# Optimization experiments

Hardware: AMD Instinct MI355X
Metric: run time of the kernel (lower is better)

The kernel has to match this reference:

```python
import jax, jax.numpy as jnp
import numpy as np

B, L, DIN = 2048, 70, 15
HID, NF, K = 16, 4, 40          # hidden_units//2, n_features, kernel_size
C = DIN + 1 + NF                # 20 signature input channels (original + time + conv features)
Z0 = 64
SIG_CH = C + C * C + C ** 3     # 8420, depth-3 signature channels


def setup_inputs() -> dict:
    key = jax.random.key(0)
    ks = jax.random.split(key, 8)
    return {
        "observed_data": jax.random.normal(ks[0], (B, L, DIN), jnp.float32),
        "observed_tp": jnp.linspace(0.0, 1.0, L, dtype=jnp.float32),
        "conv1_w": jax.random.normal(ks[1], (HID, DIN, K), jnp.float32) / np.float32(np.sqrt(DIN * K)),
        "conv1_b": jnp.zeros((HID,), jnp.float32),
        "conv2_w": jax.random.normal(ks[2], (HID, HID), jnp.float32) / np.float32(np.sqrt(HID)),
        "conv2_b": jnp.zeros((HID,), jnp.float32),
        "conv3_w": jax.random.normal(ks[3], (NF, HID), jnp.float32) / np.float32(np.sqrt(HID)),
        "conv3_b": jnp.zeros((NF,), jnp.float32),
        "w_out": jax.random.normal(ks[4], (2 * Z0, SIG_CH), jnp.float32) * np.float32(np.sqrt(2.0 / (SIG_CH + 2 * Z0))),
        "b_out": jnp.zeros((2 * Z0,), jnp.float32),
    }


def _augment(x, w1, b1, w2, b2, w3, b3):
    # x: (B, L, DIN).  signatory.Augment: conv(K) -> relu -> conv1x1 -> relu -> conv1x1,
    # then concat [truncated original, time channel, conv features] along channels.
    xc = jnp.transpose(x, (0, 2, 1))                                   # (B, DIN, L)
    h = jax.lax.conv_general_dilated(xc, w1, (1,), 'VALID')            # (B, HID, Lp)
    h = h + b1[None, :, None]
    h = jnp.einsum('oc,bcl->bol', w2, jax.nn.relu(h)) + b2[None, :, None]
    h = jnp.einsum('oc,bcl->bol', w3, jax.nn.relu(h)) + b3[None, :, None]
    conv_out = jnp.transpose(h, (0, 2, 1))                             # (B, Lp, NF)
    Lp = conv_out.shape[1]
    orig = x[:, K - 1:, :]                                             # (B, Lp, DIN)
    t = jnp.linspace(0.0, 1.0, Lp, dtype=x.dtype)
    time = jnp.broadcast_to(t[None, :, None], (x.shape[0], Lp, 1))
    return jnp.concatenate([orig, time, conv_out], axis=2)             # (B, Lp, C)


def _signature_depth3(path):
    # Truncated (depth 3) path signature with basepoint=True, via Chen's identity:
    # S <- S \otimes exp(dx) over increments, zero basepoint prepended.
    incs = jnp.diff(path, axis=1, prepend=jnp.zeros_like(path[:, :1]))  # (B, Lp, C)
    incs = jnp.transpose(incs, (1, 0, 2))                               # (Lp, B, C)
    Bn, Cn = path.shape[0], path.shape[2]
    s1 = jnp.zeros((Bn, Cn), path.dtype)
    s2 = jnp.zeros((Bn, Cn, Cn), path.dtype)
    s3 = jnp.zeros((Bn, Cn, Cn, Cn), path.dtype)

    def step(carry, d):
        s1, s2, s3 = carry
        e2 = 0.5 * d[:, :, None] * d[:, None, :]                        # d\otimes d / 2
        e3 = (e2[:, :, :, None] * d[:, None, None, :]) / 3.0            # d^{\otimes 3} / 6
        n3 = (s3
              + s2[:, :, :, None] * d[:, None, None, :]
              + s1[:, :, None, None] * e2[:, None, :, :]
              + e3)
        n2 = s2 + s1[:, :, None] * d[:, None, :] + e2
        n1 = s1 + d
        return (n1, n2, n3), None

    (s1, s2, s3), _ = jax.lax.scan(step, (s1, s2, s3), incs)
    return jnp.concatenate([s1, s2.reshape(Bn, -1), s3.reshape(Bn, -1)], axis=1)


def reference(observed_data, observed_tp, conv1_w, conv1_b, conv2_w, conv2_b,
              conv3_w, conv3_b, w_out, b_out):
    # encode_obs_time=False -> observed_tp unused
    path = _augment(observed_data, conv1_w, conv1_b, conv2_w, conv2_b, conv3_w, conv3_b)
    sig = _signature_depth3(path)                                       # (B, SIG_CH)
    z = sig @ w_out.T + b_out                                           # (B, 2*Z0)
    mean_z0 = z[:, :Z0][None]                                           # (1, B, Z0)
    std_z0 = jax.nn.softplus(z[:, Z0:][None])                           # (1, B, Z0)
    return mean_z0, std_z0
```

## Files before the change

### kernel.cpp

```cpp
#include <hip/hip_runtime.h>
#include <math.h>

#define B_TOT 2048
#define D_INC 15
#define KW    40
#define CCH   20
#define LP    31
#define SIGCH 8420
#define SIGP  8448
#define NOUT  128
#define KSPLIT 8
#define KLEN  1056

typedef _Float16 f16;
typedef _Float16 f16x8 __attribute__((ext_vector_type(8)));
typedef _Float16 f16x4 __attribute__((ext_vector_type(4)));
typedef float    f32x4 __attribute__((ext_vector_type(4)));

__global__ __launch_bounds__(256) void k_augment(
    const float* __restrict__ x,  const float* __restrict__ w1, const float* __restrict__ b1,
    const float* __restrict__ w2, const float* __restrict__ b2,
    const float* __restrict__ w3, const float* __restrict__ b3,
    float* __restrict__ path)
{
    __shared__ float xs[4 * 1068];
    __shared__ float w1s[9600];
    __shared__ float wsmall[356];
    float* w2s = wsmall;        float* b2s = wsmall + 256;
    float* w3s = wsmall + 272;  float* b3s = wsmall + 336;
    float* b1s = wsmall + 340;
    float* h1s = w1s;

    const int tid = threadIdx.x;
    const int b0  = blockIdx.x * 4;

    for (int i = tid; i < 4 * 1050; i += 256) {
        int bl = i / 1050; int t = i - bl * 1050;
        xs[bl * 1068 + t] = x[(size_t)b0 * 1050 + i];
    }
    for (int i = tid; i < 9600; i += 256) {
        int h = i / 600; int m = i - h * 600;
        w1s[m * 16 + h] = w1[i];
    }
    if (tid < 256) w2s[tid] = w2[tid];
    if (tid < 16)  b2s[tid] = b2[tid];
    if (tid < 64)  w3s[tid] = w3[tid];
    if (tid < 4)   b3s[tid] = b3[tid];
    if (tid < 16)  b1s[tid] = b1[tid];
    __syncthreads();

    const int h     = tid & 15;
    const int qr    = (tid >> 4) & 3;
    const int bl    = tid >> 6;
    const int pbase = qr * 8;

    float acc[8];
#pragma unroll
    for (int p = 0; p < 8; ++p) acc[p] = 0.f;

    for (int c = 0; c < D_INC; ++c) {
        float xcol[47];
        const int base = bl * 1068 + pbase * 15 + c;
#pragma unroll
        for (int i = 0; i < 47; ++i) xcol[i] = xs[base + i * 15];
#pragma unroll
        for (int k = 0; k < KW; ++k) {
            const float wv = w1s[(c * 40 + k) * 16 + h];
#pragma unroll
            for (int p = 0; p < 8; ++p) acc[p] += xcol[p + k] * wv;
        }
    }
    __syncthreads();
    const float bb1 = b1s[h];
#pragma unroll
    for (int p = 0; p < 8; ++p) {
        int pos = pbase + p;
        if (pos < LP) h1s[(bl * 31 + pos) * 17 + h] = fmaxf(acc[p] + bb1, 0.f);
    }
    __syncthreads();

    if (tid < 124) {
        const int bl2 = tid / 31;
        const int pos = tid - bl2 * 31;
        float hr[16];
#pragma unroll
        for (int c2 = 0; c2 < 16; ++c2) hr[c2] = h1s[tid * 17 + c2];
        float h2[16];
#pragma unroll
        for (int o = 0; o < 16; ++o) {
            float s = b2s[o];
#pragma unroll
            for (int c2 = 0; c2 < 16; ++c2) s += w2s[o * 16 + c2] * hr[c2];
            h2[o] = fmaxf(s, 0.f);
        }
        float h3[4];
#pragma unroll
        for (int f = 0; f < 4; ++f) {
            float s = b3s[f];
#pragma unroll
            for (int c2 = 0; c2 < 16; ++c2) s += w3s[f * 16 + c2] * h2[c2];
            h3[f] = s;
        }
        float* pr = path + ((size_t)(b0 + bl2) * LP + pos) * CCH;
#pragma unroll
        for (int d = 0; d < D_INC; ++d) pr[d] = xs[bl2 * 1068 + (pos + 39) * 15 + d];
        pr[15] = (float)pos * (1.0f / 30.0f);
#pragma unroll
        for (int f = 0; f < 4; ++f) pr[16 + f] = h3[f];
    }
}

__global__ __launch_bounds__(256) void k_convw(const float* __restrict__ w_out,
                                               f16* __restrict__ wh)
{
    int idx = blockIdx.x * 256 + threadIdx.x;
    int o   = idx / SIGP;
    int c   = idx - o * SIGP;
    wh[idx] = (c < SIGCH) ? (f16)w_out[(size_t)o * SIGCH + c] : (f16)0.f;
}

__global__ __launch_bounds__(256) void k_signature(const float* __restrict__ path,
                                                   f16* __restrict__ sig)
{
    __shared__ float pprev[4][656];
    __shared__ float incs[4][624];
    const int tid  = threadIdx.x;
    const int lane = tid & 63;
    const int w    = tid >> 6;
    const int b    = blockIdx.x * 4 + w;
    const float* pb = path + (size_t)b * 620;

    for (int i = lane; i < 620; i += 64) {
        float cur  = pb[i];
        float prev = (i >= 20) ? pb[i - 20] : 0.f;
        pprev[w][20 + i] = cur;
        incs[w][i] = cur - prev;
    }
    if (lane < 20) pprev[w][lane] = 0.f;
    __syncthreads();

    int iv[7], jv[7];
#pragma unroll
    for (int q = 0; q < 7; ++q) {
        int p = lane + 64 * q;
        iv[q] = p / 20; jv[q] = p - iv[q] * 20;
    }
    float s2r[7];
    float s3r[7][20];
#pragma unroll
    for (int q = 0; q < 7; ++q) {
        s2r[q] = 0.f;
#pragma unroll
        for (int k = 0; k < 20; ++k) s3r[q][k] = 0.f;
    }

    for (int t = 0; t < LP; ++t) {
        const float* ip = &incs[w][t * 20];
        const float* sp = &pprev[w][t * 20];
        float dreg[20];
        const float4* dp = (const float4*)ip;
#pragma unroll
        for (int r = 0; r < 5; ++r) {
            float4 v = dp[r];
            dreg[4 * r] = v.x; dreg[4 * r + 1] = v.y; dreg[4 * r + 2] = v.z; dreg[4 * r + 3] = v.w;
        }
#pragma unroll
        for (int q = 0; q < 7; ++q) {
            if (lane + 64 * q < 400) {
                const float di  = ip[iv[q]];
                const float dj  = ip[jv[q]];
                const float s1i = sp[iv[q]];
                const float t2  = s2r[q] + (0.5f * s1i + (1.0f / 6.0f) * di) * dj;
#pragma unroll
                for (int k = 0; k < 20; ++k) s3r[q][k] += t2 * dreg[k];
                s2r[q] += (s1i + 0.5f * di) * dj;
            }
        }
    }

    f16* sg = sig + (size_t)b * SIGP;
    if (lane < 20) sg[lane] = (f16)pprev[w][620 + lane];
#pragma unroll
    for (int q = 0; q < 6; ++q) sg[20 + q * 64 + lane] = (f16)s2r[q];
    if (lane < 16) sg[404 + lane] = (f16)s2r[6];
#pragma unroll
    for (int q = 0; q < 7; ++q) {
        int p = lane + 64 * q;
        if (p < 400) {
            f16* base = sg + 420 + p * 20;
#pragma unroll
            for (int g = 0; g < 5; ++g) {
                f16x4 v = { (f16)s3r[q][4 * g],     (f16)s3r[q][4 * g + 1],
                            (f16)s3r[q][4 * g + 2], (f16)s3r[q][4 * g + 3] };
                *(f16x4*)(base + 4 * g) = v;
            }
        }
    }
    if (lane < 28) sg[SIGCH + lane] = (f16)0.f;
}

__global__ __launch_bounds__(256) void k_gemm(const f16* __restrict__ sigh,
                                              const f16* __restrict__ wh,
                                              float* __restrict__ z_part)
{
    __shared__ f16 As[4 * 32 * 8];
    __shared__ f16 Bs[4 * 128 * 8];
    const int tid = threadIdx.x;
    const int l   = tid & 63;
    const int wv  = tid >> 6;
    const int mt  = blockIdx.x >> 3;
    const int s   = blockIdx.x & 7;
    const int m0  = mt * 32;
    const int kb  = s * KLEN;

    const f32x4 z4 = {0.f, 0.f, 0.f, 0.f};
    f32x4 acc[2][2];
    acc[0][0] = z4; acc[0][1] = z4; acc[1][0] = z4; acc[1][1] = z4;

    const size_t gA = (size_t)(m0 + (tid & 31)) * SIGP + (tid >> 5) * 8;
    const size_t gB0 = (size_t)(tid & 127) * SIGP + (tid >> 7) * 8;
    const size_t gB1 = (size_t)((256 + tid) & 127) * SIGP + ((256 + tid) >> 7) * 8;

    f16x8 aR = {}, bR0, bR1;
    if (tid < 128) aR = *(const f16x8*)(sigh + gA + kb);
    bR0 = *(const f16x8*)(wh + gB0 + kb);
    bR1 = *(const f16x8*)(wh + gB1 + kb);

    const int kg   = l >> 4;
    const int mrow = l & 15;

    for (int ch = 0; ch < 33; ++ch) {
        if (tid < 128) *(f16x8*)&As[tid * 8] = aR;
        *(f16x8*)&Bs[tid * 8] = bR0;
        *(f16x8*)&Bs[(256 + tid) * 8] = bR1;
        __syncthreads();

        if (ch < 32) {
            int k1 = kb + (ch + 1) * 32;
            if (tid < 128) aR = *(const f16x8*)(sigh + gA + k1);
            bR0 = *(const f16x8*)(wh + gB0 + k1);
            bR1 = *(const f16x8*)(wh + gB1 + k1);
        }

        f16x8 aF[2], bF[2];
#pragma unroll
        for (int m2 = 0; m2 < 2; ++m2)
            aF[m2] = *(const f16x8*)&As[(kg * 32 + m2 * 16 + mrow) * 8];
#pragma unroll
        for (int n2 = 0; n2 < 2; ++n2)
            bF[n2] = *(const f16x8*)&Bs[(kg * 128 + wv * 32 + n2 * 16 + mrow) * 8];
#pragma unroll
        for (int m2 = 0; m2 < 2; ++m2)
#pragma unroll
            for (int n2 = 0; n2 < 2; ++n2)
                acc[m2][n2] = __builtin_amdgcn_mfma_f32_16x16x32_f16(aF[m2], bF[n2], acc[m2][n2], 0, 0, 0);
        __syncthreads();
    }

#pragma unroll
    for (int m2 = 0; m2 < 2; ++m2) {
#pragma unroll
        for (int n2 = 0; n2 < 2; ++n2) {
            int n = wv * 32 + n2 * 16 + (l & 15);
#pragma unroll
            for (int r = 0; r < 4; ++r) {
                int m = m0 + m2 * 16 + (l >> 4) * 4 + r;
                z_part[((size_t)s * B_TOT + m) * NOUT + n] = acc[m2][n2][r];
            }
        }
    }
}

__global__ __launch_bounds__(256) void k_final(const float* __restrict__ z_part,
                                               const float* __restrict__ b_out,
                                               float* __restrict__ out)
{
    int idx = blockIdx.x * 256 + threadIdx.x;
    int b = idx >> 7;
    int o = idx & 127;
    float z = b_out[o];
#pragma unroll
    for (int s = 0; s < KSPLIT; ++s) z += z_part[((size_t)s * B_TOT + b) * NOUT + o];
    if (o < 64) {
        out[(size_t)b * 64 + o] = z;
    } else {
        float sp = fmaxf(z, 0.f) + log1pf(expf(-fabsf(z)));
        out[131072 + (size_t)b * 64 + (o - 64)] = sp;
    }
}

extern "C" void kernel_launch(void* const* d_in, const int* in_sizes, int n_in,
                              void* d_out, int out_size, void* d_ws, size_t ws_size,
                              hipStream_t stream)
{
    const float* x     = (const float*)d_in[0];
    const float* w1    = (const float*)d_in[2];
    const float* b1    = (const float*)d_in[3];
    const float* w2    = (const float*)d_in[4];
    const float* b2    = (const float*)d_in[5];
    const float* w3    = (const float*)d_in[6];
    const float* b3    = (const float*)d_in[7];
    const float* w_out = (const float*)d_in[8];
    const float* b_out = (const float*)d_in[9];
    float* out = (float*)d_out;

    float* ws   = (float*)d_ws;
    float* path = ws;
    f16*   sigh = (f16*)(ws + 1269760);
    f16*   wh   = (f16*)(ws + 9920512);
    float* zpart = ws + 10461184;

    hipLaunchKernelGGL(k_augment,   dim3(512),  dim3(256), 0, stream,
                       x, w1, b1, w2, b2, w3, b3, path);
    hipLaunchKernelGGL(k_convw,     dim3(4224), dim3(256), 0, stream, w_out, wh);
    hipLaunchKernelGGL(k_signature, dim3(512),  dim3(256), 0, stream, path, sigh);
    hipLaunchKernelGGL(k_gemm,      dim3(512),  dim3(256), 0, stream, sigh, wh, zpart);
    hipLaunchKernelGGL(k_final,     dim3(1024), dim3(256), 0, stream, zpart, b_out, out);
}
```

Baseline: 161.9 us.

## Fuse augment, signature and weight conversion into one kernel; retile GEMM K-split

The augment, weight-conversion and signature kernels are merged into one launch. The augmented path stays in shared memory instead of going through global memory, and 32 extra blocks convert w_out to fp16 with vectorized loads. The GEMM now uses 11 K-splits of 768 with a 64-wide K chunk per stage, which gives 704 blocks and fewer barriers. This removes two launches and a global path round-trip, at the cost of more shared memory reuse in the fused kernel and more partial sums for the final reduction.

After: 158.6 us. 1.02x faster.

```diff
diff --git a/kernel.cpp b/kernel.cpp
--- a/kernel.cpp
+++ b/kernel.cpp
@@ -9,27 +9,54 @@
 #define SIGCH 8420
 #define SIGP  8448
 #define NOUT  128
-#define KSPLIT 8
-#define KLEN  1056
+#define KSPLIT 11
+#define KLEN  768
 
 typedef _Float16 f16;
 typedef _Float16 f16x8 __attribute__((ext_vector_type(8)));
 typedef _Float16 f16x4 __attribute__((ext_vector_type(4)));
 typedef float    f32x4 __attribute__((ext_vector_type(4)));
 
-__global__ __launch_bounds__(256) void k_augment(
+__global__ __launch_bounds__(256) void k_augsig(
     const float* __restrict__ x,  const float* __restrict__ w1, const float* __restrict__ b1,
     const float* __restrict__ w2, const float* __restrict__ b2,
     const float* __restrict__ w3, const float* __restrict__ b3,
-    float* __restrict__ path)
+    const float* __restrict__ w_out, f16* __restrict__ wh, f16* __restrict__ sig)
 {
+    if (blockIdx.x >= 512) {
+        int t0 = (blockIdx.x - 512) * 256 + threadIdx.x;
+        for (int chunk = t0; chunk < 128 * 1056; chunk += 8192) {
+            int o  = chunk / 1056;
+            int cw = chunk - o * 1056;
+            int c0 = cw * 8;
+            f16x8 v;
+            if (c0 + 8 <= SIGCH) {
+                const float* src = w_out + (size_t)o * SIGCH + c0;
+                float4 a = *(const float4*)src;
+                float4 b = *(const float4*)(src + 4);
+                v = (f16x8){(f16)a.x,(f16)a.y,(f16)a.z,(f16)a.w,
+                            (f16)b.x,(f16)b.y,(f16)b.z,(f16)b.w};
+            } else {
+#pragma unroll
+                for (int e = 0; e < 8; ++e) {
+                    int c = c0 + e;
+                    v[e] = (c < SIGCH) ? (f16)w_out[(size_t)o * SIGCH + c] : (f16)0.f;
+                }
+            }
+            *(f16x8*)(wh + (size_t)o * SIGP + c0) = v;
+        }
+        return;
+    }
+
     __shared__ float xs[4 * 1068];
     __shared__ float w1s[9600];
     __shared__ float wsmall[356];
     float* w2s = wsmall;        float* b2s = wsmall + 256;
     float* w3s = wsmall + 272;  float* b3s = wsmall + 336;
     float* b1s = wsmall + 340;
-    float* h1s = w1s;
+    float* h1s   = w1s;
+    float* pprev = w1s + 2624;
+    float* incs  = w1s + 5248;
 
     const int tid = threadIdx.x;
     const int b0  = blockIdx.x * 4;
@@ -49,35 +76,35 @@
     if (tid < 16)  b1s[tid] = b1[tid];
     __syncthreads();
 
-    const int h     = tid & 15;
-    const int qr    = (tid >> 4) & 3;
-    const int bl    = tid >> 6;
-    const int pbase = qr * 8;
-
-    float acc[8];
-#pragma unroll
-    for (int p = 0; p < 8; ++p) acc[p] = 0.f;
-
-    for (int c = 0; c < D_INC; ++c) {
-        float xcol[47];
-        const int base = bl * 1068 + pbase * 15 + c;
-#pragma unroll
-        for (int i = 0; i < 47; ++i) xcol[i] = xs[base + i * 15];
-#pragma unroll
-        for (int k = 0; k < KW; ++k) {
-            const float wv = w1s[(c * 40 + k) * 16 + h];
-#pragma unroll
-            for (int p = 0; p < 8; ++p) acc[p] += xcol[p + k] * wv;
-        }
-    }
-    __syncthreads();
-    const float bb1 = b1s[h];
-#pragma unroll
-    for (int p = 0; p < 8; ++p) {
-        int pos = pbase + p;
-        if (pos < LP) h1s[(bl * 31 + pos) * 17 + h] = fmaxf(acc[p] + bb1, 0.f);
-    }
-    __syncthreads();
+    {
+        const int h     = tid & 15;
+        const int qr    = (tid >> 4) & 3;
+        const int bl    = tid >> 6;
+        const int pbase = qr * 8;
+        float acc[8];
+#pragma unroll
+        for (int p = 0; p < 8; ++p) acc[p] = 0.f;
+        for (int c = 0; c < D_INC; ++c) {
+            float xcol[47];
+            const int base = bl * 1068 + pbase * 15 + c;
+#pragma unroll
+            for (int i = 0; i < 47; ++i) xcol[i] = xs[base + i * 15];
+#pragma unroll
+            for (int k = 0; k < KW; ++k) {
+                const float wv = w1s[(c * 40 + k) * 16 + h];
+#pragma unroll
+                for (int p = 0; p < 8; ++p) acc[p] += xcol[p + k] * wv;
+            }
+        }
+        __syncthreads();
+        const float bb1 = b1s[h];
+#pragma unroll
+        for (int p = 0; p < 8; ++p) {
+            int pos = pbase + p;
+            if (pos < LP) h1s[(bl * 31 + pos) * 17 + h] = fmaxf(acc[p] + bb1, 0.f);
+        }
+        __syncthreads();
+    }
 
     if (tid < 124) {
         const int bl2 = tid / 31;
@@ -101,42 +128,25 @@
             for (int c2 = 0; c2 < 16; ++c2) s += w3s[f * 16 + c2] * h2[c2];
             h3[f] = s;
         }
-        float* pr = path + ((size_t)(b0 + bl2) * LP + pos) * CCH;
+        float* pr = pprev + bl2 * 656 + 20 + pos * 20;
 #pragma unroll
         for (int d = 0; d < D_INC; ++d) pr[d] = xs[bl2 * 1068 + (pos + 39) * 15 + d];
         pr[15] = (float)pos * (1.0f / 30.0f);
 #pragma unroll
         for (int f = 0; f < 4; ++f) pr[16 + f] = h3[f];
-    }
-}
-
-__global__ __launch_bounds__(256) void k_convw(const float* __restrict__ w_out,
-                                               f16* __restrict__ wh)
-{
-    int idx = blockIdx.x * 256 + threadIdx.x;
-    int o   = idx / SIGP;
-    int c   = idx - o * SIGP;
-    wh[idx] = (c < SIGCH) ? (f16)w_out[(size_t)o * SIGCH + c] : (f16)0.f;
-}
-
-__global__ __launch_bounds__(256) void k_signature(const float* __restrict__ path,
-                                                   f16* __restrict__ sig)
-{
-    __shared__ float pprev[4][656];
-    __shared__ float incs[4][624];
-    const int tid  = threadIdx.x;
+    } else {
+        int z = tid - 124;
+        if (z < 80) pprev[(z / 20) * 656 + (z % 20)] = 0.f;
+    }
+    __syncthreads();
+
     const int lane = tid & 63;
     const int w    = tid >> 6;
-    const int b    = blockIdx.x * 4 + w;
-    const float* pb = path + (size_t)b * 620;
-
-    for (int i = lane; i < 620; i += 64) {
-        float cur  = pb[i];
-        float prev = (i >= 20) ? pb[i - 20] : 0.f;
-        pprev[w][20 + i] = cur;
-        incs[w][i] = cur - prev;
-    }
-    if (lane < 20) pprev[w][lane] = 0.f;
+    const int b    = b0 + w;
+    float* pp = pprev + w * 656;
+    float* ic = incs  + w * 624;
+
+    for (int i = lane; i < 620; i += 64) ic[i] = pp[20 + i] - pp[i];
     __syncthreads();
 
     int iv[7], jv[7];
@@ -155,14 +165,14 @@
     }
 
     for (int t = 0; t < LP; ++t) {
-        const float* ip = &incs[w][t * 20];
-        const float* sp = &pprev[w][t * 20];
+        const float* ip = &ic[t * 20];
+        const float* sp = &pp[t * 20];
         float dreg[20];
         const float4* dp = (const float4*)ip;
 #pragma unroll
         for (int r = 0; r < 5; ++r) {
             float4 v = dp[r];
-            dreg[4 * r] = v.x; dreg[4 * r + 1] = v.y; dreg[4 * r + 2] = v.z; dreg[4 * r + 3] = v.w;
+            dreg[4*r] = v.x; dreg[4*r+1] = v.y; dreg[4*r+2] = v.z; dreg[4*r+3] = v.w;
         }
 #pragma unroll
         for (int q = 0; q < 7; ++q) {
@@ -179,7 +189,7 @@
     }
 
     f16* sg = sig + (size_t)b * SIGP;
-    if (lane < 20) sg[lane] = (f16)pprev[w][620 + lane];
+    if (lane < 20) sg[lane] = (f16)pp[620 + lane];
 #pragma unroll
     for (int q = 0; q < 6; ++q) sg[20 + q * 64 + lane] = (f16)s2r[q];
     if (lane < 16) sg[404 + lane] = (f16)s2r[6];
@@ -190,8 +200,8 @@
             f16* base = sg + 420 + p * 20;
 #pragma unroll
             for (int g = 0; g < 5; ++g) {
-                f16x4 v = { (f16)s3r[q][4 * g],     (f16)s3r[q][4 * g + 1],
-                            (f16)s3r[q][4 * g + 2], (f16)s3r[q][4 * g + 3] };
+                f16x4 v = { (f16)s3r[q][4*g],   (f16)s3r[q][4*g+1],
+                            (f16)s3r[q][4*g+2], (f16)s3r[q][4*g+3] };
                 *(f16x4*)(base + 4 * g) = v;
             }
         }
@@ -203,13 +213,13 @@
                                               const f16* __restrict__ wh,
                                               float* __restrict__ z_part)
 {
-    __shared__ f16 As[4 * 32 * 8];
-    __shared__ f16 Bs[4 * 128 * 8];
+    __shared__ f16 As[2048];
+    __shared__ f16 Bs[8192];
     const int tid = threadIdx.x;
     const int l   = tid & 63;
     const int wv  = tid >> 6;
-    const int mt  = blockIdx.x >> 3;
-    const int s   = blockIdx.x & 7;
+    const int mt  = blockIdx.x / KSPLIT;
+    const int s   = blockIdx.x - mt * KSPLIT;
     const int m0  = mt * 32;
     const int kb  = s * KLEN;
 
@@ -217,43 +227,50 @@
     f32x4 acc[2][2];
     acc[0][0] = z4; acc[0][1] = z4; acc[1][0] = z4; acc[1][1] = z4;
 
-    const size_t gA = (size_t)(m0 + (tid & 31)) * SIGP + (tid >> 5) * 8;
-    const size_t gB0 = (size_t)(tid & 127) * SIGP + (tid >> 7) * 8;
-    const size_t gB1 = (size_t)((256 + tid) & 127) * SIGP + ((256 + tid) >> 7) * 8;
-
-    f16x8 aR = {}, bR0, bR1;
-    if (tid < 128) aR = *(const f16x8*)(sigh + gA + kb);
-    bR0 = *(const f16x8*)(wh + gB0 + kb);
-    bR1 = *(const f16x8*)(wh + gB1 + kb);
+    const size_t gA = (size_t)(m0 + (tid & 31)) * SIGP + kb + (tid >> 5) * 8;
+    size_t gB[4];
+#pragma unroll
+    for (int r = 0; r < 4; ++r) {
+        int slot = r * 256 + tid;
+        gB[r] = (size_t)(slot & 127) * SIGP + kb + (slot >> 7) * 8;
+    }
+
+    f16x8 aR = *(const f16x8*)(sigh + gA);
+    f16x8 bR[4];
+#pragma unroll
+    for (int r = 0; r < 4; ++r) bR[r] = *(const f16x8*)(wh + gB[r]);
 
     const int kg   = l >> 4;
     const int mrow = l & 15;
 
-    for (int ch = 0; ch < 33; ++ch) {
-        if (tid < 128) *(f16x8*)&As[tid * 8] = aR;
-        *(f16x8*)&Bs[tid * 8] = bR0;
-        *(f16x8*)&Bs[(256 + tid) * 8] = bR1;
+    for (int ch = 0; ch < 12; ++ch) {
+        *(f16x8*)&As[tid * 8] = aR;
+#pragma unroll
+        for (int r = 0; r < 4; ++r) *(f16x8*)&Bs[(r * 256 + tid) * 8] = bR[r];
         __syncthreads();
 
-        if (ch < 32) {
-            int k1 = kb + (ch + 1) * 32;
-            if (tid < 128) aR = *(const f16x8*)(sigh + gA + k1);
-            bR0 = *(const f16x8*)(wh + gB0 + k1);
-            bR1 = *(const f16x8*)(wh + gB1 + k1);
-        }
-
-        f16x8 aF[2], bF[2];
-#pragma unroll
-        for (int m2 = 0; m2 < 2; ++m2)
-            aF[m2] = *(const f16x8*)&As[(kg * 32 + m2 * 16 + mrow) * 8];
-#pragma unroll
-        for (int n2 = 0; n2 < 2; ++n2)
-            bF[n2] = *(const f16x8*)&Bs[(kg * 128 + wv * 32 + n2 * 16 + mrow) * 8];
-#pragma unroll
-        for (int m2 = 0; m2 < 2; ++m2)
+        if (ch < 11) {
+            int koff = (ch + 1) * 64;
+            aR = *(const f16x8*)(sigh + gA + koff);
+#pragma unroll
+            for (int r = 0; r < 4; ++r) bR[r] = *(const f16x8*)(wh + gB[r] + koff);
+        }
+
+#pragma unroll
+        for (int kc = 0; kc < 2; ++kc) {
+            f16x8 aF[2], bF[2];
+#pragma unroll
+            for (int m2 = 0; m2 < 2; ++m2)
+                aF[m2] = *(const f16x8*)&As[((kc * 4 + kg) * 32 + m2 * 16 + mrow) * 8];
 #pragma unroll
             for (int n2 = 0; n2 < 2; ++n2)
-                acc[m2][n2] = __builtin_amdgcn_mfma_f32_16x16x32_f16(aF[m2], bF[n2], acc[m2][n2], 0, 0, 0);
+                bF[n2] = *(const f16x8*)&Bs[((kc * 4 + kg) * 128 + wv * 32 + n2 * 16 + mrow) * 8];
+#pragma unroll
+            for (int m2 = 0; m2 < 2; ++m2)
+#pragma unroll
+                for (int n2 = 0; n2 < 2; ++n2)
+                    acc[m2][n2] = __builtin_amdgcn_mfma_f32_16x16x32_f16(aF[m2], bF[n2], acc[m2][n2], 0, 0, 0);
+        }
         __syncthreads();
     }
 
@@ -304,16 +321,13 @@
     const float* b_out = (const float*)d_in[9];
     float* out = (float*)d_out;
 
-    float* ws   = (float*)d_ws;
-    float* path = ws;
-    f16*   sigh = (f16*)(ws + 1269760);
-    f16*   wh   = (f16*)(ws + 9920512);
-    float* zpart = ws + 10461184;
-
-    hipLaunchKernelGGL(k_augment,   dim3(512),  dim3(256), 0, stream,
-                       x, w1, b1, w2, b2, w3, b3, path);
-    hipLaunchKernelGGL(k_convw,     dim3(4224), dim3(256), 0, stream, w_out, wh);
-    hipLaunchKernelGGL(k_signature, dim3(512),  dim3(256), 0, stream, path, sigh);
-    hipLaunchKernelGGL(k_gemm,      dim3(512),  dim3(256), 0, stream, sigh, wh, zpart);
-    hipLaunchKernelGGL(k_final,     dim3(1024), dim3(256), 0, stream, zpart, b_out, out);
+    float* ws    = (float*)d_ws;
+    f16*   sigh  = (f16*)ws;
+    f16*   wh    = (f16*)(ws + 8650752);
+    float* zpart = ws + 9191424;
+
+    hipLaunchKernelGGL(k_augsig, dim3(544),  dim3(256), 0, stream,
+                       x, w1, b1, w2, b2, w3, b3, w_out, wh, sigh);
+    hipLaunchKernelGGL(k_gemm,   dim3(704),  dim3(256), 0, stream, sigh, wh, zpart);
+    hipLaunchKernelGGL(k_final,  dim3(1024), dim3(256), 0, stream, zpart, b_out, out);
 }
```
